# Kernel optimization log

Hardware: AMD Instinct MI355X
Metric: run time of the kernel (lower is better)

## Reference

```python
import jax, jax.numpy as jnp
import numpy as np

N = 100000   # nodes
E = 1600000  # edges
D = 128      # state_dim
H1 = 512
H2 = 256


def setup_inputs() -> dict:
    key = jax.random.key(0)
    ks = jax.random.split(key, 8)
    x = jax.random.normal(ks[0], (N, D), jnp.float32)
    edge_index = jax.random.randint(ks[1], (2, E), 0, N, dtype=jnp.int64)
    W_gcn = jax.random.normal(ks[2], (D, D), jnp.float32) * (1.0 / np.sqrt(D))
    b_gcn = jnp.zeros((D,), jnp.float32)
    W1 = jax.random.normal(ks[3], (D, H1), jnp.float32) * (1.0 / np.sqrt(D))
    b1 = jnp.zeros((H1,), jnp.float32)
    W2 = jax.random.normal(ks[4], (H1, H2), jnp.float32) * (1.0 / np.sqrt(H1))
    b2 = jnp.zeros((H2,), jnp.float32)
    W3 = jax.random.normal(ks[5], (H2, 1), jnp.float32) * (1.0 / np.sqrt(H2))
    b3 = jnp.zeros((1,), jnp.float32)
    return {"x": x, "edge_index": edge_index, "W_gcn": W_gcn, "b_gcn": b_gcn,
            "W1": W1, "b1": b1, "W2": W2, "b2": b2, "W3": W3, "b3": b3}


def _gcn_conv(x, edge_index, W, b):
    # PyG GCNConv: linear transform, add self-loops, symmetric deg^-1/2 norm,
    # scatter-sum messages from src to dst, add bias.
    n = x.shape[0]
    loop = jnp.arange(n, dtype=edge_index.dtype)
    src = jnp.concatenate([edge_index[0], loop])
    dst = jnp.concatenate([edge_index[1], loop])
    deg = jax.ops.segment_sum(jnp.ones_like(dst, x.dtype), dst, num_segments=n)
    dinv = jnp.where(deg > 0, jax.lax.rsqrt(jnp.maximum(deg, 1e-12)), 0.0)
    norm = dinv[src] * dinv[dst]                      # [E+N]
    h = x @ W                                         # [N, D]
    msg = h[src] * norm[:, None]                      # gather + scale
    out = jax.ops.segment_sum(msg, dst, num_segments=n)  # scatter-add
    return out + b


def reference(x, edge_index, W_gcn, b_gcn, W1, b1, W2, b2, W3, b3):
    out = jax.nn.relu(_gcn_conv(x, edge_index, W_gcn, b_gcn))
    h = out + x                                       # residual
    h = jax.nn.relu(h @ W1 + b1)
    h = jax.nn.relu(h @ W2 + b2)                      # dropout is identity in eval
    return h @ W3 + b3                                # [N, 1]
```

## Files before the change

### kernel.cpp

```cpp
#include <hip/hip_runtime.h>

#define DN  128
#define H1N 512
#define H2N 256
#define TILE_A 4096
#define BKT_CAP 6144

typedef __attribute__((ext_vector_type(8))) short short8_t;
typedef __attribute__((ext_vector_type(4))) float f32x4;

__device__ inline ushort f2bf(float f) {
  union { float f; unsigned u; } v; v.f = f;
  unsigned r = v.u + 0x7FFF + ((v.u >> 16) & 1);
  return (ushort)(r >> 16);
}
__device__ inline float asf(unsigned u) {
  union { unsigned u; float f; } v; v.u = u;
  return v.f;
}


__global__ __launch_bounds__(256) void k_bucketA(const int* __restrict__ ei,
                                                 int* __restrict__ bcur,
                                                 uint2* __restrict__ pairs,
                                                 int E, int NB) {
  __shared__ int hist[512];
  __shared__ int start[512];
  __shared__ int cur[512];
  __shared__ int gbase[512];
  __shared__ uint2 lp[TILE_A];
  int t = threadIdx.x;
  int base = blockIdx.x * TILE_A;
  int cnt = E - base; if (cnt > TILE_A) cnt = TILE_A;

  for (int i = t; i < 512; i += 256) hist[i] = 0;
  __syncthreads();

  int sreg[16], dreg[16];
#pragma unroll
  for (int k = 0; k < 16; ++k) {
    int idx = t + 256 * k;
    bool v = idx < cnt;
    sreg[k] = v ? ei[base + idx] : 0;
    dreg[k] = v ? ei[E + base + idx] : -1;
    if (v) atomicAdd(&hist[dreg[k] >> 8], 1);
  }
  __syncthreads();

  for (int i = t; i < 512; i += 256) start[i] = hist[i];
  __syncthreads();
  for (int o = 1; o < 512; o <<= 1) {
    int i0 = t, i1 = t + 256;
    int v0 = (i0 >= o) ? start[i0 - o] : 0;
    int v1 = (i1 >= o) ? start[i1 - o] : 0;
    __syncthreads();
    start[i0] += v0;
    start[i1] += v1;
    __syncthreads();
  }
  for (int i = t; i < 512; i += 256) start[i] -= hist[i];
  __syncthreads();
  for (int i = t; i < 512; i += 256) cur[i] = start[i];
  __syncthreads();

#pragma unroll
  for (int k = 0; k < 16; ++k) {
    if (dreg[k] >= 0) {
      int d = dreg[k] >> 8;
      int p = atomicAdd(&cur[d], 1);
      lp[p] = make_uint2((unsigned)sreg[k], (unsigned)dreg[k]);
    }
  }
  __syncthreads();

  for (int i = t; i < NB; i += 256)
    gbase[i] = hist[i] ? atomicAdd(&bcur[i], hist[i]) : 0;
  __syncthreads();

  for (int p = t; p < cnt; p += 256) {
    uint2 pr = lp[p];
    int d = (int)(pr.y >> 8);
    int o = gbase[d] + (p - start[d]);
    if (o < BKT_CAP) pairs[(size_t)d * BKT_CAP + o] = pr;
  }
}


__global__ __launch_bounds__(256) void k_bucketB(const uint2* __restrict__ pairs,
                                                 const int* __restrict__ bcur,
                                                 int* __restrict__ csr,
                                                 int* __restrict__ ro,
                                                 int* __restrict__ re,
                                                 float* __restrict__ dinv,
                                                 int N) {
  __shared__ int hist[256];
  __shared__ int cur[256];
  __shared__ int lout[BKT_CAP];
  __shared__ uint2 lp[BKT_CAP];
  int b = blockIdx.x, t = threadIdx.x;
  size_t p0 = (size_t)b * BKT_CAP;
  int cnt = bcur[b]; if (cnt > BKT_CAP) cnt = BKT_CAP;

  hist[t] = 0;
  __syncthreads();
  for (int k = t; k < cnt; k += 256) {
    uint2 pr = pairs[p0 + k];
    lp[k] = pr;
    atomicAdd(&hist[pr.y & 255u], 1);
  }
  __syncthreads();

  int v = hist[t];
  cur[t] = v; __syncthreads();
  for (int o = 1; o < 256; o <<= 1) {
    int a = (t >= o) ? cur[t - o] : 0;
    __syncthreads();
    cur[t] += a;
    __syncthreads();
  }
  int excl = cur[t] - v;
  int node = (b << 8) + t;
  if (node < N) {
    ro[node] = (int)p0 + excl;
    re[node] = (int)p0 + excl + v;
    dinv[node] = rsqrtf((float)(v + 1));
  }
  __syncthreads();
  cur[t] = excl;
  __syncthreads();

  for (int k = t; k < cnt; k += 256) {
    uint2 pr = lp[k];
    int p = atomicAdd(&cur[(int)(pr.y & 255u)], 1);
    lout[p] = (int)pr.x;
  }
  __syncthreads();
  for (int k = t; k < cnt; k += 256) csr[p0 + k] = lout[k];
}


__device__ inline void pack_one(int idx, const float* __restrict__ W,
                                ushort* __restrict__ Wp, int K, int Ncols) {
  int ksn = K >> 5;
  int l  = idx & 63;
  int ks = (idx >> 6) % ksn;
  int ct = idx / (64 * ksn);
  int col = ct * 16 + (l & 15);
  int kb  = ks * 32 + (l >> 4) * 8;
  short8_t v;
#pragma unroll
  for (int r = 0; r < 8; ++r)
    v[r] = (short)f2bf(W[(size_t)(kb + r) * Ncols + col]);
  *(short8_t*)&Wp[(size_t)idx * 8] = v;
}

__global__ __launch_bounds__(256) void k_packall(const float* __restrict__ Wg,
                                                 const float* __restrict__ W1,
                                                 const float* __restrict__ W2,
                                                 ushort* __restrict__ Wgp,
                                                 ushort* __restrict__ W1p,
                                                 ushort* __restrict__ W2p) {
  int idx = blockIdx.x * 256 + threadIdx.x;
  if (idx < 2048)        pack_one(idx, Wg, Wgp, DN, DN);
  else if (idx < 10240)  pack_one(idx - 2048, W1, W1p, DN, H1N);
  else if (idx < 26624)  pack_one(idx - 10240, W2, W2p, H1N, H2N);
}


__global__ __launch_bounds__(256, 4) void k_gemm1(const float* __restrict__ x,
                                                  const ushort* __restrict__ Wgp,
                                                  const float* __restrict__ dinv,
                                                  ushort* __restrict__ hs, int N) {
  __shared__ ushort xT[64 * 128];
  int t = threadIdx.x;
  int row0 = blockIdx.x * 64;

#pragma unroll
  for (int i = 0; i < 4; ++i) {
    int c = t + 256 * i;
    int r = c >> 4, d0 = (c & 15) * 8;
    int gr = row0 + r;
    float4 v0 = {0,0,0,0}, v1 = {0,0,0,0};
    if (gr < N) {
      v0 = *(const float4*)(x + (size_t)gr * DN + d0);
      v1 = *(const float4*)(x + (size_t)gr * DN + d0 + 4);
    }
    short8_t p;
    p[0]=(short)f2bf(v0.x); p[1]=(short)f2bf(v0.y); p[2]=(short)f2bf(v0.z); p[3]=(short)f2bf(v0.w);
    p[4]=(short)f2bf(v1.x); p[5]=(short)f2bf(v1.y); p[6]=(short)f2bf(v1.z); p[7]=(short)f2bf(v1.w);
    *(short8_t*)((char*)xT + r * 256 + ((d0 * 2) ^ ((r & 7) << 4))) = p;
  }
  __syncthreads();

  int w = t >> 6, l = t & 63;
  int lr = l & 15, lk = l >> 4;
  const short8_t* pbg = (const short8_t*)Wgp;

  f32x4 acc[4][2];
#pragma unroll
  for (int mf = 0; mf < 4; ++mf)
#pragma unroll
    for (int n = 0; n < 2; ++n) acc[mf][n] = (f32x4){0.f,0.f,0.f,0.f};

  auto g_load = [&](short8_t (&bb)[2], int ks) {
#pragma unroll
    for (int n = 0; n < 2; ++n)
      bb[n] = pbg[((w * 2 + n) * 4 + ks) * 64 + l];
  };
  auto g_mfma = [&](short8_t (&bb)[2], int ks) {
    short8_t a[4];
#pragma unroll
    for (int mf = 0; mf < 4; ++mf) {
      int r = mf * 16 + lr;
      a[mf] = *(const short8_t*)((const char*)xT + r * 256 + ((ks * 64 + lk * 16) ^ ((r & 7) << 4)));
    }
#pragma unroll
    for (int mf = 0; mf < 4; ++mf)
#pragma unroll
      for (int n = 0; n < 2; ++n)
        acc[mf][n] = __builtin_amdgcn_mfma_f32_16x16x32_bf16(a[mf], bb[n], acc[mf][n], 0, 0, 0);
  };

  short8_t bA[2], bB[2];
  g_load(bA, 0);
  g_load(bB, 1); g_mfma(bA, 0);
  g_load(bA, 2); g_mfma(bB, 1);
  g_load(bB, 3); g_mfma(bA, 2);
  g_mfma(bB, 3);

  float dv[4][4];
#pragma unroll
  for (int mf = 0; mf < 4; ++mf)
#pragma unroll
    for (int r2 = 0; r2 < 4; ++r2) {
      int gr = row0 + mf * 16 + lk * 4 + r2;
      dv[mf][r2] = (gr < N) ? dinv[gr] : 0.f;
    }
#pragma unroll
  for (int n = 0; n < 2; ++n) {
    int col = (w * 2 + n) * 16 + lr;
#pragma unroll
    for (int mf = 0; mf < 4; ++mf)
#pragma unroll
      for (int r2 = 0; r2 < 4; ++r2) {
        int gr = row0 + mf * 16 + lk * 4 + r2;
        if (gr < N) hs[(size_t)gr * DN + col] = f2bf(acc[mf][n][r2] * dv[mf][r2]);
      }
  }
}


__global__ __launch_bounds__(256) void k_agg(const ushort* __restrict__ hs,
                                             const float* __restrict__ x,
                                             const int* __restrict__ csr,
                                             const int* __restrict__ ro,
                                             const int* __restrict__ re,
                                             const float* __restrict__ dinv,
                                             const float* __restrict__ bg,
                                             ushort* __restrict__ aggb, int N) {
  int t = threadIdx.x;
  int node = blockIdx.x * 16 + (t >> 4);
  if (node >= N) return;
  int d0 = (t & 15) * 8;

  int beg = ro[node], end = re[node];
  float dn = dinv[node];
  uint4 selfv = *(const uint4*)(hs + (size_t)node * DN + d0);
  float4 x0 = *(const float4*)(x + (size_t)node * DN + d0);
  float4 x1 = *(const float4*)(x + (size_t)node * DN + d0 + 4);
  float4 b0 = *(const float4*)(bg + d0);
  float4 b1v = *(const float4*)(bg + d0 + 4);

  float s[8];
#pragma unroll
  for (int i = 0; i < 8; ++i) s[i] = 0.f;

  auto accum = [&](uint4 v) {
    s[0] += asf(v.x << 16); s[1] += asf(v.x & 0xffff0000u);
    s[2] += asf(v.y << 16); s[3] += asf(v.y & 0xffff0000u);
    s[4] += asf(v.z << 16); s[5] += asf(v.z & 0xffff0000u);
    s[6] += asf(v.w << 16); s[7] += asf(v.w & 0xffff0000u);
  };

  int e = beg;
  for (; e + 4 <= end; e += 4) {
    int i0 = csr[e], i1 = csr[e + 1], i2 = csr[e + 2], i3 = csr[e + 3];
    uint4 v0 = *(const uint4*)(hs + (size_t)i0 * DN + d0);
    uint4 v1 = *(const uint4*)(hs + (size_t)i1 * DN + d0);
    uint4 v2 = *(const uint4*)(hs + (size_t)i2 * DN + d0);
    uint4 v3 = *(const uint4*)(hs + (size_t)i3 * DN + d0);
    accum(v0); accum(v1); accum(v2); accum(v3);
  }
  if (e + 2 <= end) {
    int i0 = csr[e], i1 = csr[e + 1];
    uint4 v0 = *(const uint4*)(hs + (size_t)i0 * DN + d0);
    uint4 v1 = *(const uint4*)(hs + (size_t)i1 * DN + d0);
    accum(v0); accum(v1);
    e += 2;
  }
  if (e < end) {
    int i0 = csr[e];
    accum(*(const uint4*)(hs + (size_t)i0 * DN + d0));
  }
  accum(selfv);

  float xv[8] = {x0.x, x0.y, x0.z, x0.w, x1.x, x1.y, x1.z, x1.w};
  float bv[8] = {b0.x, b0.y, b0.z, b0.w, b1v.x, b1v.y, b1v.z, b1v.w};
  uint outp[4];
#pragma unroll
  for (int i = 0; i < 4; ++i) {
    ushort lo = f2bf(fmaxf(s[2*i]   * dn + bv[2*i],   0.f) + xv[2*i]);
    ushort hi = f2bf(fmaxf(s[2*i+1] * dn + bv[2*i+1], 0.f) + xv[2*i+1]);
    outp[i] = (uint)lo | ((uint)hi << 16);
  }
  *(uint4*)(aggb + (size_t)node * DN + d0) = *(uint4*)outp;
}


__global__ __launch_bounds__(512, 2) void k_mlp(const ushort* __restrict__ aggb,
                                                const ushort* __restrict__ W1p,
                                                const float* __restrict__ b1,
                                                const ushort* __restrict__ W2p,
                                                const float* __restrict__ b2,
                                                const float* __restrict__ W3,
                                                const float* __restrict__ b3,
                                                float* __restrict__ out, int N) {
  __shared__ ushort aT[64 * 128];
  __shared__ ushort t1[64 * 512];
  int t = threadIdx.x;
  int row0 = blockIdx.x * 64;

#pragma unroll
  for (int i = 0; i < 2; ++i) {
    int c = t + 512 * i;
    int r = c >> 4;
    int cb = (c & 15) * 16;
    int gr = row0 + r;
    uint4 v = {0, 0, 0, 0};
    if (gr < N) v = *(const uint4*)(aggb + (size_t)gr * DN + (c & 15) * 8);
    *(uint4*)((char*)aT + r * 256 + (cb ^ ((r & 7) << 4))) = v;
  }
  __syncthreads();

  int w = t >> 6, l = t & 63;
  int lr = l & 15, lk = l >> 4;

  const short8_t* pb1 = (const short8_t*)W1p;
  f32x4 acc1[4][4];
#pragma unroll
  for (int mf = 0; mf < 4; ++mf)
#pragma unroll
    for (int n = 0; n < 4; ++n) acc1[mf][n] = (f32x4){0.f,0.f,0.f,0.f};

  auto s1_load = [&](short8_t (&bb)[4], int ks) {
#pragma unroll
    for (int n = 0; n < 4; ++n)
      bb[n] = pb1[((w * 4 + n) * 4 + ks) * 64 + l];
  };
  auto s1_mfma = [&](short8_t (&bb)[4], int ks) {
    short8_t a[4];
#pragma unroll
    for (int mf = 0; mf < 4; ++mf) {
      int r = mf * 16 + lr;
      a[mf] = *(const short8_t*)((const char*)aT + r * 256 + ((ks * 64 + lk * 16) ^ ((r & 7) << 4)));
    }
#pragma unroll
    for (int mf = 0; mf < 4; ++mf)
#pragma unroll
      for (int n = 0; n < 4; ++n)
        acc1[mf][n] = __builtin_amdgcn_mfma_f32_16x16x32_bf16(a[mf], bb[n], acc1[mf][n], 0, 0, 0);
  };

  {
    short8_t bA[4], bB[4];
    s1_load(bA, 0);
    s1_load(bB, 1); s1_mfma(bA, 0);
    s1_load(bA, 2); s1_mfma(bB, 1);
    s1_load(bB, 3); s1_mfma(bA, 2);
    s1_mfma(bB, 3);
  }

#pragma unroll
  for (int n = 0; n < 4; ++n) {
    int col = (w * 4 + n) * 16 + lr;
    float bb = b1[col];
#pragma unroll
    for (int mf = 0; mf < 4; ++mf)
#pragma unroll
      for (int r2 = 0; r2 < 4; ++r2) {
        int rr = mf * 16 + lk * 4 + r2;
        *(ushort*)((char*)t1 + rr * 1024 + ((col * 2) ^ ((rr & 7) << 4))) =
            f2bf(fmaxf(acc1[mf][n][r2] + bb, 0.f));
      }
  }
  __syncthreads();

  const short8_t* pb2 = (const short8_t*)W2p;
  f32x4 acc2[4][2];
#pragma unroll
  for (int mf = 0; mf < 4; ++mf)
#pragma unroll
    for (int n = 0; n < 2; ++n) acc2[mf][n] = (f32x4){0.f,0.f,0.f,0.f};

  auto s2_load = [&](short8_t (&bb)[4], int p) {
#pragma unroll
    for (int n = 0; n < 2; ++n) {
      bb[n]     = pb2[((w * 2 + n) * 16 + 2 * p)     * 64 + l];
      bb[2 + n] = pb2[((w * 2 + n) * 16 + 2 * p + 1) * 64 + l];
    }
  };
  auto s2_mfma = [&](short8_t (&bb)[4], int p) {
#pragma unroll
    for (int h = 0; h < 2; ++h) {
      int ks = 2 * p + h;
      short8_t a[4];
#pragma unroll
      for (int mf = 0; mf < 4; ++mf) {
        int r = mf * 16 + lr;
        a[mf] = *(const short8_t*)((const char*)t1 + r * 1024 + ((ks * 64 + lk * 16) ^ ((r & 7) << 4)));
      }
#pragma unroll
      for (int mf = 0; mf < 4; ++mf)
#pragma unroll
        for (int n = 0; n < 2; ++n)
          acc2[mf][n] = __builtin_amdgcn_mfma_f32_16x16x32_bf16(a[mf], bb[2 * h + n], acc2[mf][n], 0, 0, 0);
    }
  };

  {
    short8_t c0[4], c1[4], c2[4];
    s2_load(c0, 0); s2_load(c1, 1);
    s2_load(c2, 2); s2_mfma(c0, 0);
    s2_load(c0, 3); s2_mfma(c1, 1);
    s2_load(c1, 4); s2_mfma(c2, 2);
    s2_load(c2, 5); s2_mfma(c0, 3);
    s2_load(c0, 6); s2_mfma(c1, 4);
    s2_load(c1, 7); s2_mfma(c2, 5);
    s2_mfma(c0, 6);
    s2_mfma(c1, 7);
  }

  float po[4][4];
#pragma unroll
  for (int mf = 0; mf < 4; ++mf)
#pragma unroll
    for (int r2 = 0; r2 < 4; ++r2) po[mf][r2] = 0.f;
#pragma unroll
  for (int n = 0; n < 2; ++n) {
    int col = (w * 2 + n) * 16 + lr;
    float bb = b2[col];
    float w3 = W3[col];
#pragma unroll
    for (int mf = 0; mf < 4; ++mf)
#pragma unroll
      for (int r2 = 0; r2 < 4; ++r2)
        po[mf][r2] += fmaxf(acc2[mf][n][r2] + bb, 0.f) * w3;
  }
#pragma unroll
  for (int mf = 0; mf < 4; ++mf)
#pragma unroll
    for (int r2 = 0; r2 < 4; ++r2) {
      float v = po[mf][r2];
      v += __shfl_xor(v, 1, 64);
      v += __shfl_xor(v, 2, 64);
      v += __shfl_xor(v, 4, 64);
      v += __shfl_xor(v, 8, 64);
      po[mf][r2] = v;
    }
  float* pf = (float*)aT;
  if (lr == 0) {
#pragma unroll
    for (int mf = 0; mf < 4; ++mf)
#pragma unroll
      for (int r2 = 0; r2 < 4; ++r2)
        pf[w * 64 + mf * 16 + lk * 4 + r2] = po[mf][r2];
  }
  __syncthreads();
  if (t < 64) {
    int gr = row0 + t;
    if (gr < N) {
      float s = b3[0];
#pragma unroll
      for (int ww = 0; ww < 8; ++ww) s += pf[ww * 64 + t];
      out[gr] = s;
    }
  }
}


extern "C" void kernel_launch(void* const* d_in, const int* in_sizes, int n_in,
                              void* d_out, int out_size, void* d_ws, size_t ws_size,
                              hipStream_t stream) {
  const float* x  = (const float*)d_in[0];
  const int*   ei = (const int*)d_in[1];
  const float* Wg = (const float*)d_in[2];
  const float* bg = (const float*)d_in[3];
  const float* W1 = (const float*)d_in[4];
  const float* b1 = (const float*)d_in[5];
  const float* W2 = (const float*)d_in[6];
  const float* b2 = (const float*)d_in[7];
  const float* W3 = (const float*)d_in[8];
  const float* b3 = (const float*)d_in[9];
  float* out = (float*)d_out;

  const int N = in_sizes[0] / DN;
  const int E = in_sizes[1] / 2;
  const int NB = (N + 255) >> 8;

  char* ws = (char*)d_ws;
  size_t off = 0;
  auto alloc = [&](size_t bytes) -> void* {
    void* p = ws + off;
    off = (off + bytes + 255) & ~(size_t)255;
    return p;
  };
  int*    bcur   = (int*)alloc((size_t)NB * 4);
  int*    ro     = (int*)alloc((size_t)N * 4);
  int*    re     = (int*)alloc((size_t)N * 4);
  float*  dinv   = (float*)alloc((size_t)N * 4);
  int*    csr    = (int*)alloc((size_t)NB * BKT_CAP * 4);
  uint2*  pairs  = (uint2*)alloc((size_t)NB * BKT_CAP * 8);
  ushort* hsb    = (ushort*)alloc((size_t)N * DN * 2);
  ushort* aggb   = (ushort*)alloc((size_t)N * DN * 2);
  ushort* Wgp    = (ushort*)alloc((size_t)DN * DN * 2);
  ushort* W1p    = (ushort*)alloc((size_t)DN * H1N * 2);
  ushort* W2p    = (ushort*)alloc((size_t)H1N * H2N * 2);
  (void)ws_size; (void)n_in; (void)out_size;

  hipMemsetAsync(bcur, 0, (size_t)NB * 4, stream);

  int nTiles = (E + TILE_A - 1) / TILE_A;
  k_bucketA<<<nTiles, 256, 0, stream>>>(ei, bcur, pairs, E, NB);
  k_bucketB<<<NB, 256, 0, stream>>>(pairs, bcur, csr, ro, re, dinv, N);

  k_packall<<<104, 256, 0, stream>>>(Wg, W1, W2, Wgp, W1p, W2p);

  int nb64 = (N + 63) / 64;
  k_gemm1<<<nb64, 256, 0, stream>>>(x, Wgp, dinv, hsb, N);
  k_agg<<<(N + 15) / 16, 256, 0, stream>>>(hsb, x, csr, ro, re, dinv, bg, aggb, N);
  k_mlp<<<nb64, 512, 0, stream>>>(aggb, W1p, b1, W2p, b2, W3, b3, out, N);
}
```

Before: 192.3 us.

## Pack edge pairs into 32 bits and move residual add into MLP via bf16 x

Edge (src,dst) pairs are packed into one 32-bit word (src<<8 | dst&255), with the bucket id kept in a separate shared ushort array. This halves the global pairs buffer traffic between the two bucketing kernels. The residual x is also written as bf16 by the first GEMM and added in the MLP load stage rather than read as fp32 in the aggregation kernel. That trades an fp32 x read in agg for a bf16 write plus a bf16 read, and adds an extra bf16 rounding of the sum. The packing requires src < 2^24.

Result: no change. 193.2 us (+0.5%).

```diff
diff --git a/kernel.cpp b/kernel.cpp
--- a/kernel.cpp
+++ b/kernel.cpp
@@ -22,13 +22,14 @@
 
 __global__ __launch_bounds__(256) void k_bucketA(const int* __restrict__ ei,
                                                  int* __restrict__ bcur,
-                                                 uint2* __restrict__ pairs,
+                                                 uint* __restrict__ pairs,
                                                  int E, int NB) {
   __shared__ int hist[512];
   __shared__ int start[512];
   __shared__ int cur[512];
   __shared__ int gbase[512];
-  __shared__ uint2 lp[TILE_A];
+  __shared__ uint lp[TILE_A];
+  __shared__ ushort bid[TILE_A];
   int t = threadIdx.x;
   int base = blockIdx.x * TILE_A;
   int cnt = E - base; if (cnt > TILE_A) cnt = TILE_A;
@@ -68,7 +69,8 @@
     if (dreg[k] >= 0) {
       int d = dreg[k] >> 8;
       int p = atomicAdd(&cur[d], 1);
-      lp[p] = make_uint2((unsigned)sreg[k], (unsigned)dreg[k]);
+      lp[p]  = ((uint)sreg[k] << 8) | ((uint)dreg[k] & 255u);
+      bid[p] = (ushort)d;
     }
   }
   __syncthreads();
@@ -78,15 +80,14 @@
   __syncthreads();
 
   for (int p = t; p < cnt; p += 256) {
-    uint2 pr = lp[p];
-    int d = (int)(pr.y >> 8);
+    int d = bid[p];
     int o = gbase[d] + (p - start[d]);
-    if (o < BKT_CAP) pairs[(size_t)d * BKT_CAP + o] = pr;
-  }
-}
-
-
-__global__ __launch_bounds__(256) void k_bucketB(const uint2* __restrict__ pairs,
+    if (o < BKT_CAP) pairs[(size_t)d * BKT_CAP + o] = lp[p];
+  }
+}
+
+
+__global__ __launch_bounds__(256) void k_bucketB(const uint* __restrict__ pairs,
                                                  const int* __restrict__ bcur,
                                                  int* __restrict__ csr,
                                                  int* __restrict__ ro,
@@ -96,7 +97,7 @@
   __shared__ int hist[256];
   __shared__ int cur[256];
   __shared__ int lout[BKT_CAP];
-  __shared__ uint2 lp[BKT_CAP];
+  __shared__ uint lp[BKT_CAP];
   int b = blockIdx.x, t = threadIdx.x;
   size_t p0 = (size_t)b * BKT_CAP;
   int cnt = bcur[b]; if (cnt > BKT_CAP) cnt = BKT_CAP;
@@ -104,9 +105,9 @@
   hist[t] = 0;
   __syncthreads();
   for (int k = t; k < cnt; k += 256) {
-    uint2 pr = pairs[p0 + k];
+    uint pr = pairs[p0 + k];
     lp[k] = pr;
-    atomicAdd(&hist[pr.y & 255u], 1);
+    atomicAdd(&hist[pr & 255u], 1);
   }
   __syncthreads();
 
@@ -130,9 +131,9 @@
   __syncthreads();
 
   for (int k = t; k < cnt; k += 256) {
-    uint2 pr = lp[k];
-    int p = atomicAdd(&cur[(int)(pr.y & 255u)], 1);
-    lout[p] = (int)pr.x;
+    uint pr = lp[k];
+    int p = atomicAdd(&cur[(int)(pr & 255u)], 1);
+    lout[p] = (int)(pr >> 8);
   }
   __syncthreads();
   for (int k = t; k < cnt; k += 256) csr[p0 + k] = lout[k];
@@ -170,7 +171,8 @@
 __global__ __launch_bounds__(256, 4) void k_gemm1(const float* __restrict__ x,
                                                   const ushort* __restrict__ Wgp,
                                                   const float* __restrict__ dinv,
-                                                  ushort* __restrict__ hs, int N) {
+                                                  ushort* __restrict__ hs,
+                                                  ushort* __restrict__ xb, int N) {
   __shared__ ushort xT[64 * 128];
   int t = threadIdx.x;
   int row0 = blockIdx.x * 64;
@@ -188,6 +190,7 @@
     short8_t p;
     p[0]=(short)f2bf(v0.x); p[1]=(short)f2bf(v0.y); p[2]=(short)f2bf(v0.z); p[3]=(short)f2bf(v0.w);
     p[4]=(short)f2bf(v1.x); p[5]=(short)f2bf(v1.y); p[6]=(short)f2bf(v1.z); p[7]=(short)f2bf(v1.w);
+    if (gr < N) *(short8_t*)(xb + (size_t)gr * DN + d0) = p;
     *(short8_t*)((char*)xT + r * 256 + ((d0 * 2) ^ ((r & 7) << 4))) = p;
   }
   __syncthreads();
@@ -251,7 +254,6 @@
 
 
 __global__ __launch_bounds__(256) void k_agg(const ushort* __restrict__ hs,
-                                             const float* __restrict__ x,
                                              const int* __restrict__ csr,
                                              const int* __restrict__ ro,
                                              const int* __restrict__ re,
@@ -266,8 +268,6 @@
   int beg = ro[node], end = re[node];
   float dn = dinv[node];
   uint4 selfv = *(const uint4*)(hs + (size_t)node * DN + d0);
-  float4 x0 = *(const float4*)(x + (size_t)node * DN + d0);
-  float4 x1 = *(const float4*)(x + (size_t)node * DN + d0 + 4);
   float4 b0 = *(const float4*)(bg + d0);
   float4 b1v = *(const float4*)(bg + d0 + 4);
 
@@ -304,13 +304,12 @@
   }
   accum(selfv);
 
-  float xv[8] = {x0.x, x0.y, x0.z, x0.w, x1.x, x1.y, x1.z, x1.w};
   float bv[8] = {b0.x, b0.y, b0.z, b0.w, b1v.x, b1v.y, b1v.z, b1v.w};
   uint outp[4];
 #pragma unroll
   for (int i = 0; i < 4; ++i) {
-    ushort lo = f2bf(fmaxf(s[2*i]   * dn + bv[2*i],   0.f) + xv[2*i]);
-    ushort hi = f2bf(fmaxf(s[2*i+1] * dn + bv[2*i+1], 0.f) + xv[2*i+1]);
+    ushort lo = f2bf(fmaxf(s[2*i]   * dn + bv[2*i],   0.f));
+    ushort hi = f2bf(fmaxf(s[2*i+1] * dn + bv[2*i+1], 0.f));
     outp[i] = (uint)lo | ((uint)hi << 16);
   }
   *(uint4*)(aggb + (size_t)node * DN + d0) = *(uint4*)outp;
@@ -318,6 +317,7 @@
 
 
 __global__ __launch_bounds__(512, 2) void k_mlp(const ushort* __restrict__ aggb,
+                                                const ushort* __restrict__ xb,
                                                 const ushort* __restrict__ W1p,
                                                 const float* __restrict__ b1,
                                                 const ushort* __restrict__ W2p,
@@ -334,11 +334,22 @@
   for (int i = 0; i < 2; ++i) {
     int c = t + 512 * i;
     int r = c >> 4;
-    int cb = (c & 15) * 16;
+    int d0 = (c & 15) * 8;
     int gr = row0 + r;
-    uint4 v = {0, 0, 0, 0};
-    if (gr < N) v = *(const uint4*)(aggb + (size_t)gr * DN + (c & 15) * 8);
-    *(uint4*)((char*)aT + r * 256 + (cb ^ ((r & 7) << 4))) = v;
+    uint4 va = {0, 0, 0, 0}, vx = {0, 0, 0, 0};
+    if (gr < N) {
+      va = *(const uint4*)(aggb + (size_t)gr * DN + d0);
+      vx = *(const uint4*)(xb   + (size_t)gr * DN + d0);
+    }
+    uint outp[4];
+#pragma unroll
+    for (int j = 0; j < 4; ++j) {
+      uint a = ((const uint*)&va)[j], b = ((const uint*)&vx)[j];
+      float lo = asf(a << 16) + asf(b << 16);
+      float hi = asf(a & 0xffff0000u) + asf(b & 0xffff0000u);
+      outp[j] = (uint)f2bf(lo) | ((uint)f2bf(hi) << 16);
+    }
+    *(uint4*)((char*)aT + r * 256 + ((d0 * 2) ^ ((r & 7) << 4))) = *(uint4*)outp;
   }
   __syncthreads();
 
@@ -519,9 +530,10 @@
   int*    re     = (int*)alloc((size_t)N * 4);
   float*  dinv   = (float*)alloc((size_t)N * 4);
   int*    csr    = (int*)alloc((size_t)NB * BKT_CAP * 4);
-  uint2*  pairs  = (uint2*)alloc((size_t)NB * BKT_CAP * 8);
+  uint*   pairs  = (uint*)alloc((size_t)NB * BKT_CAP * 4);
   ushort* hsb    = (ushort*)alloc((size_t)N * DN * 2);
   ushort* aggb   = (ushort*)alloc((size_t)N * DN * 2);
+  ushort* xbb    = (ushort*)alloc((size_t)N * DN * 2);
   ushort* Wgp    = (ushort*)alloc((size_t)DN * DN * 2);
   ushort* W1p    = (ushort*)alloc((size_t)DN * H1N * 2);
   ushort* W2p    = (ushort*)alloc((size_t)H1N * H2N * 2);
@@ -536,7 +548,7 @@
   k_packall<<<104, 256, 0, stream>>>(Wg, W1, W2, Wgp, W1p, W2p);
 
   int nb64 = (N + 63) / 64;
-  k_gemm1<<<nb64, 256, 0, stream>>>(x, Wgp, dinv, hsb, N);
-  k_agg<<<(N + 15) / 16, 256, 0, stream>>>(hsb, x, csr, ro, re, dinv, bg, aggb, N);
-  k_mlp<<<nb64, 512, 0, stream>>>(aggb, W1p, b1, W2p, b2, W3, b3, out, N);
-}
+  k_gemm1<<<nb64, 256, 0, stream>>>(x, Wgp, dinv, hsb, xbb, N);
+  k_agg<<<(N + 15) / 16, 256, 0, stream>>>(hsb, csr, ro, re, dinv, bg, aggb, N);
+  k_mlp<<<nb64, 512, 0, stream>>>(aggb, xbb, W1p, b1, W2p, b2, W3, b3, out, N);
+}
```

## Pack edge pairs into 32-bit words and transpose MLP MFMA operands

Applied to the files above, without the earlier changes.

The bucketing stage now packs each edge as (src<<8 | dst&255) in a single 32-bit word, with the bucket id kept in a separate shared ushort array. This halves the global pairs buffer traffic and the shared-memory footprint, but it relies on src fitting in 24 bits. The fused MLP kernel swaps the MFMA operand order so each lane's accumulator holds four consecutive output columns. That lets the bias+ReLU epilogue write packed ushort4 stores and load biases as vectors, and it cuts the final reduction shuffles from four to two per value. The second-layer pipeline is also restructured to load one k-step of weights at a time.

Result: no change. 188.8 us (-1.8%).

```diff
diff --git a/kernel.cpp b/kernel.cpp
--- a/kernel.cpp
+++ b/kernel.cpp
@@ -22,13 +22,14 @@
 
 __global__ __launch_bounds__(256) void k_bucketA(const int* __restrict__ ei,
                                                  int* __restrict__ bcur,
-                                                 uint2* __restrict__ pairs,
+                                                 uint* __restrict__ pairs,
                                                  int E, int NB) {
   __shared__ int hist[512];
   __shared__ int start[512];
   __shared__ int cur[512];
   __shared__ int gbase[512];
-  __shared__ uint2 lp[TILE_A];
+  __shared__ uint lp[TILE_A];
+  __shared__ ushort bid[TILE_A];
   int t = threadIdx.x;
   int base = blockIdx.x * TILE_A;
   int cnt = E - base; if (cnt > TILE_A) cnt = TILE_A;
@@ -68,7 +69,8 @@
     if (dreg[k] >= 0) {
       int d = dreg[k] >> 8;
       int p = atomicAdd(&cur[d], 1);
-      lp[p] = make_uint2((unsigned)sreg[k], (unsigned)dreg[k]);
+      lp[p]  = ((uint)sreg[k] << 8) | ((uint)dreg[k] & 255u);
+      bid[p] = (ushort)d;
     }
   }
   __syncthreads();
@@ -78,15 +80,14 @@
   __syncthreads();
 
   for (int p = t; p < cnt; p += 256) {
-    uint2 pr = lp[p];
-    int d = (int)(pr.y >> 8);
+    int d = bid[p];
     int o = gbase[d] + (p - start[d]);
-    if (o < BKT_CAP) pairs[(size_t)d * BKT_CAP + o] = pr;
-  }
-}
-
-
-__global__ __launch_bounds__(256) void k_bucketB(const uint2* __restrict__ pairs,
+    if (o < BKT_CAP) pairs[(size_t)d * BKT_CAP + o] = lp[p];
+  }
+}
+
+
+__global__ __launch_bounds__(256) void k_bucketB(const uint* __restrict__ pairs,
                                                  const int* __restrict__ bcur,
                                                  int* __restrict__ csr,
                                                  int* __restrict__ ro,
@@ -96,7 +97,7 @@
   __shared__ int hist[256];
   __shared__ int cur[256];
   __shared__ int lout[BKT_CAP];
-  __shared__ uint2 lp[BKT_CAP];
+  __shared__ uint lp[BKT_CAP];
   int b = blockIdx.x, t = threadIdx.x;
   size_t p0 = (size_t)b * BKT_CAP;
   int cnt = bcur[b]; if (cnt > BKT_CAP) cnt = BKT_CAP;
@@ -104,9 +105,9 @@
   hist[t] = 0;
   __syncthreads();
   for (int k = t; k < cnt; k += 256) {
-    uint2 pr = pairs[p0 + k];
+    uint pr = pairs[p0 + k];
     lp[k] = pr;
-    atomicAdd(&hist[pr.y & 255u], 1);
+    atomicAdd(&hist[pr & 255u], 1);
   }
   __syncthreads();
 
@@ -130,9 +131,9 @@
   __syncthreads();
 
   for (int k = t; k < cnt; k += 256) {
-    uint2 pr = lp[k];
-    int p = atomicAdd(&cur[(int)(pr.y & 255u)], 1);
-    lout[p] = (int)pr.x;
+    uint pr = lp[k];
+    int p = atomicAdd(&cur[(int)(pr & 255u)], 1);
+    lout[p] = (int)(pr >> 8);
   }
   __syncthreads();
   for (int k = t; k < cnt; k += 256) csr[p0 + k] = lout[k];
@@ -348,9 +349,9 @@
   const short8_t* pb1 = (const short8_t*)W1p;
   f32x4 acc1[4][4];
 #pragma unroll
-  for (int mf = 0; mf < 4; ++mf)
-#pragma unroll
-    for (int n = 0; n < 4; ++n) acc1[mf][n] = (f32x4){0.f,0.f,0.f,0.f};
+  for (int n = 0; n < 4; ++n)
+#pragma unroll
+    for (int mf = 0; mf < 4; ++mf) acc1[n][mf] = (f32x4){0.f,0.f,0.f,0.f};
 
   auto s1_load = [&](short8_t (&bb)[4], int ks) {
 #pragma unroll
@@ -358,17 +359,17 @@
       bb[n] = pb1[((w * 4 + n) * 4 + ks) * 64 + l];
   };
   auto s1_mfma = [&](short8_t (&bb)[4], int ks) {
-    short8_t a[4];
+    short8_t aF[4];
 #pragma unroll
     for (int mf = 0; mf < 4; ++mf) {
       int r = mf * 16 + lr;
-      a[mf] = *(const short8_t*)((const char*)aT + r * 256 + ((ks * 64 + lk * 16) ^ ((r & 7) << 4)));
-    }
-#pragma unroll
-    for (int mf = 0; mf < 4; ++mf)
-#pragma unroll
-      for (int n = 0; n < 4; ++n)
-        acc1[mf][n] = __builtin_amdgcn_mfma_f32_16x16x32_bf16(a[mf], bb[n], acc1[mf][n], 0, 0, 0);
+      aF[mf] = *(const short8_t*)((const char*)aT + r * 256 + ((ks * 64 + lk * 16) ^ ((r & 7) << 4)));
+    }
+#pragma unroll
+    for (int n = 0; n < 4; ++n)
+#pragma unroll
+      for (int mf = 0; mf < 4; ++mf)
+        acc1[n][mf] = __builtin_amdgcn_mfma_f32_16x16x32_bf16(bb[n], aF[mf], acc1[n][mf], 0, 0, 0);
   };
 
   {
@@ -382,98 +383,94 @@
 
 #pragma unroll
   for (int n = 0; n < 4; ++n) {
-    int col = (w * 4 + n) * 16 + lr;
-    float bb = b1[col];
+    f32x4 b1v = *(const f32x4*)&b1[(w * 4 + n) * 16 + lk * 4];
+#pragma unroll
+    for (int mf = 0; mf < 4; ++mf) {
+      int rr = mf * 16 + lr;
+      ushort4 pk;
+      pk.x = f2bf(fmaxf(acc1[n][mf][0] + b1v[0], 0.f));
+      pk.y = f2bf(fmaxf(acc1[n][mf][1] + b1v[1], 0.f));
+      pk.z = f2bf(fmaxf(acc1[n][mf][2] + b1v[2], 0.f));
+      pk.w = f2bf(fmaxf(acc1[n][mf][3] + b1v[3], 0.f));
+      int cb2 = ((w * 4 + n) * 32 + lk * 8) ^ ((rr & 7) << 4);
+      *(ushort4*)((char*)t1 + rr * 1024 + cb2) = pk;
+    }
+  }
+  __syncthreads();
+
+  const short8_t* pb2 = (const short8_t*)W2p;
+  f32x4 acc2[2][4];
+#pragma unroll
+  for (int n = 0; n < 2; ++n)
+#pragma unroll
+    for (int mf = 0; mf < 4; ++mf) acc2[n][mf] = (f32x4){0.f,0.f,0.f,0.f};
+
+  auto s2_load = [&](short8_t (&bb)[2], int ks) {
+#pragma unroll
+    for (int n = 0; n < 2; ++n)
+      bb[n] = pb2[((w * 2 + n) * 16 + ks) * 64 + l];
+  };
+  auto s2_mfma = [&](short8_t (&bb)[2], int ks) {
+    short8_t tF[4];
+#pragma unroll
+    for (int mf = 0; mf < 4; ++mf) {
+      int r = mf * 16 + lr;
+      tF[mf] = *(const short8_t*)((const char*)t1 + r * 1024 + ((ks * 64 + lk * 16) ^ ((r & 7) << 4)));
+    }
+#pragma unroll
+    for (int n = 0; n < 2; ++n)
+#pragma unroll
+      for (int mf = 0; mf < 4; ++mf)
+        acc2[n][mf] = __builtin_amdgcn_mfma_f32_16x16x32_bf16(bb[n], tF[mf], acc2[n][mf], 0, 0, 0);
+  };
+
+  {
+    short8_t c0[2], c1[2], c2[2];
+    s2_load(c0, 0); s2_load(c1, 1); s2_load(c2, 2);
+    s2_mfma(c0, 0);  s2_load(c0, 3);
+    s2_mfma(c1, 1);  s2_load(c1, 4);
+    s2_mfma(c2, 2);  s2_load(c2, 5);
+    s2_mfma(c0, 3);  s2_load(c0, 6);
+    s2_mfma(c1, 4);  s2_load(c1, 7);
+    s2_mfma(c2, 5);  s2_load(c2, 8);
+    s2_mfma(c0, 6);  s2_load(c0, 9);
+    s2_mfma(c1, 7);  s2_load(c1, 10);
+    s2_mfma(c2, 8);  s2_load(c2, 11);
+    s2_mfma(c0, 9);  s2_load(c0, 12);
+    s2_mfma(c1, 10); s2_load(c1, 13);
+    s2_mfma(c2, 11); s2_load(c2, 14);
+    s2_mfma(c0, 12); s2_load(c0, 15);
+    s2_mfma(c1, 13);
+    s2_mfma(c2, 14);
+    s2_mfma(c0, 15);
+  }
+
+  float po[4];
+#pragma unroll
+  for (int mf = 0; mf < 4; ++mf) po[mf] = 0.f;
+#pragma unroll
+  for (int n = 0; n < 2; ++n) {
+    int colb = (w * 2 + n) * 16 + lk * 4;
+    f32x4 b2v = *(const f32x4*)&b2[colb];
+    f32x4 w3v = *(const f32x4*)&W3[colb];
 #pragma unroll
     for (int mf = 0; mf < 4; ++mf)
 #pragma unroll
-      for (int r2 = 0; r2 < 4; ++r2) {
-        int rr = mf * 16 + lk * 4 + r2;
-        *(ushort*)((char*)t1 + rr * 1024 + ((col * 2) ^ ((rr & 7) << 4))) =
-            f2bf(fmaxf(acc1[mf][n][r2] + bb, 0.f));
-      }
-  }
-  __syncthreads();
-
-  const short8_t* pb2 = (const short8_t*)W2p;
-  f32x4 acc2[4][2];
-#pragma unroll
-  for (int mf = 0; mf < 4; ++mf)
-#pragma unroll
-    for (int n = 0; n < 2; ++n) acc2[mf][n] = (f32x4){0.f,0.f,0.f,0.f};
-
-  auto s2_load = [&](short8_t (&bb)[4], int p) {
-#pragma unroll
-    for (int n = 0; n < 2; ++n) {
-      bb[n]     = pb2[((w * 2 + n) * 16 + 2 * p)     * 64 + l];
-      bb[2 + n] = pb2[((w * 2 + n) * 16 + 2 * p + 1) * 64 + l];
-    }
-  };
-  auto s2_mfma = [&](short8_t (&bb)[4], int p) {
-#pragma unroll
-    for (int h = 0; h < 2; ++h) {
-      int ks = 2 * p + h;
-      short8_t a[4];
-#pragma unroll
-      for (int mf = 0; mf < 4; ++mf) {
-        int r = mf * 16 + lr;
-        a[mf] = *(const short8_t*)((const char*)t1 + r * 1024 + ((ks * 64 + lk * 16) ^ ((r & 7) << 4)));
-      }
-#pragma unroll
-      for (int mf = 0; mf < 4; ++mf)
-#pragma unroll
-        for (int n = 0; n < 2; ++n)
-          acc2[mf][n] = __builtin_amdgcn_mfma_f32_16x16x32_bf16(a[mf], bb[2 * h + n], acc2[mf][n], 0, 0, 0);
-    }
-  };
-
-  {
-    short8_t c0[4], c1[4], c2[4];
-    s2_load(c0, 0); s2_load(c1, 1);
-    s2_load(c2, 2); s2_mfma(c0, 0);
-    s2_load(c0, 3); s2_mfma(c1, 1);
-    s2_load(c1, 4); s2_mfma(c2, 2);
-    s2_load(c2, 5); s2_mfma(c0, 3);
-    s2_load(c0, 6); s2_mfma(c1, 4);
-    s2_load(c1, 7); s2_mfma(c2, 5);
-    s2_mfma(c0, 6);
-    s2_mfma(c1, 7);
-  }
-
-  float po[4][4];
-#pragma unroll
-  for (int mf = 0; mf < 4; ++mf)
-#pragma unroll
-    for (int r2 = 0; r2 < 4; ++r2) po[mf][r2] = 0.f;
-#pragma unroll
-  for (int n = 0; n < 2; ++n) {
-    int col = (w * 2 + n) * 16 + lr;
-    float bb = b2[col];
-    float w3 = W3[col];
+      for (int r2 = 0; r2 < 4; ++r2)
+        po[mf] += fmaxf(acc2[n][mf][r2] + b2v[r2], 0.f) * w3v[r2];
+  }
+#pragma unroll
+  for (int mf = 0; mf < 4; ++mf) {
+    float v = po[mf];
+    v += __shfl_xor(v, 16, 64);
+    v += __shfl_xor(v, 32, 64);
+    po[mf] = v;
+  }
+  float* pf = (float*)aT;
+  if (lk == 0) {
 #pragma unroll
     for (int mf = 0; mf < 4; ++mf)
-#pragma unroll
-      for (int r2 = 0; r2 < 4; ++r2)
-        po[mf][r2] += fmaxf(acc2[mf][n][r2] + bb, 0.f) * w3;
-  }
-#pragma unroll
-  for (int mf = 0; mf < 4; ++mf)
-#pragma unroll
-    for (int r2 = 0; r2 < 4; ++r2) {
-      float v = po[mf][r2];
-      v += __shfl_xor(v, 1, 64);
-      v += __shfl_xor(v, 2, 64);
-      v += __shfl_xor(v, 4, 64);
-      v += __shfl_xor(v, 8, 64);
-      po[mf][r2] = v;
-    }
-  float* pf = (float*)aT;
-  if (lr == 0) {
-#pragma unroll
-    for (int mf = 0; mf < 4; ++mf)
-#pragma unroll
-      for (int r2 = 0; r2 < 4; ++r2)
-        pf[w * 64 + mf * 16 + lk * 4 + r2] = po[mf][r2];
+      pf[w * 64 + mf * 16 + lr] = po[mf];
   }
   __syncthreads();
   if (t < 64) {
@@ -519,7 +516,7 @@
   int*    re     = (int*)alloc((size_t)N * 4);
   float*  dinv   = (float*)alloc((size_t)N * 4);
   int*    csr    = (int*)alloc((size_t)NB * BKT_CAP * 4);
-  uint2*  pairs  = (uint2*)alloc((size_t)NB * BKT_CAP * 8);
+  uint*   pairs  = (uint*)alloc((size_t)NB * BKT_CAP * 4);
   ushort* hsb    = (ushort*)alloc((size_t)N * DN * 2);
   ushort* aggb   = (ushort*)alloc((size_t)N * DN * 2);
   ushort* Wgp    = (ushort*)alloc((size_t)DN * DN * 2);
```
